# Performance work log

Measured on AMD Instinct MI355X. Metric: run time of the kernel, lower is better.

## Reference

```python
import jax, jax.numpy as jnp
import numpy as np

H, DH, DIM, BNECK, NK, COND = 8, 64, 256, 128, 32, 256


def _ln(x):
    m = x.mean(-1, keepdims=True)
    v = ((x - m) ** 2).mean(-1, keepdims=True)
    return (x - m) * jax.lax.rsqrt(v + 1e-5)


def _mlp(x, w1, b1, w2, b2):
    return jax.nn.gelu(x @ w1 + b1) @ w2 + b2


def _radial(d, w):
    # Bessel-type radial basis sin(n*d)/d projected to heads; limit n as d->0
    n = jnp.arange(1, NK + 1, dtype=d.dtype)
    safe = jnp.maximum(d, 1e-6)[..., None]
    basis = jnp.where(d[..., None] > 1e-6, jnp.sin(d[..., None] * n) / safe, n)
    return jnp.einsum('ijk,kh->hij', basis, w)


def _kernel(x, qk_w):
    # DotProductKernel with softmax=False, scale=1.0
    b, n, _ = x.shape
    qk = (x @ qk_w).reshape(b, n, 2, H, DH).transpose(0, 3, 2, 1, 4)  # b h two n d
    q, k = qk[:, :, 0], qk[:, :, 1]
    return jnp.einsum('bhid,bhjd->bhij', q, k)


def reference(u, lat, lat_diff, lon_diff, scalar_cond, adaLN_w, adaLN_b, to_v_w, to_x_in_w, to_x_w1, to_x_b1, to_x_w2, to_x_b2, to_y_in_w, to_y_w1, to_y_b1, to_y_w2, to_y_b2, kx_qk_w, ky_qk_w, rx_w, ry_w, merge_w, merge_b, ffn_w1, ffn_b1, ffn_w2, ffn_b2):
    b, nlat, nlon, c = u.shape
    mod = (scalar_cond @ adaLN_w + adaLN_b)[:, None, None]  # (b,1,1,6c)
    sh_msa, sc_msa, g_msa, sh_mlp, sc_mlp, g_mlp = jnp.split(mod, 6, axis=-1)
    u_skip = u
    um = _ln(u) * (1 + sc_msa) + sh_msa  # modulate_fused
    lw = jnp.cos(lat)
    lw = lw / lw.mean()
    # PoolingReducer over lat (weighted) -> (b, nlon, bneck)
    u_x = _mlp(jnp.einsum('bilc,cd,i->bld', um, to_x_in_w, lw) / nlat,
               to_x_w1, to_x_b1, to_x_w2, to_x_b2)
    # PoolingReducer over lon -> (b, nlat, bneck)
    u_y = _mlp((um @ to_y_in_w).mean(axis=2), to_y_w1, to_y_b1, to_y_w2, to_y_b2)
    k_x = jax.nn.softmax(_kernel(u_x, kx_qk_w) * _radial(lon_diff, rx_w)[None], axis=-1)
    k_y = jax.nn.softmax(_kernel(u_y, ky_qk_w) * _radial(lat_diff, ry_w)[None], axis=-1)
    v = (um @ to_v_w).reshape(b, nlat, nlon, H, DH).transpose(0, 3, 1, 2, 4)  # b h i l c
    u_phi = jnp.einsum('bhij,bhjmc->bhimc', k_y, v)
    u_phi = jnp.einsum('bhlm,bhimc->bhilc', k_x, u_phi)
    u_phi = u_phi.transpose(0, 2, 3, 1, 4)  # b i l h c
    mu = u_phi.mean(-1, keepdims=True)
    var = ((u_phi - mu) ** 2).mean(-1, keepdims=True)
    gn = ((u_phi - mu) * jax.lax.rsqrt(var + 1e-6)).reshape(b, nlat, nlon, H * DH)
    u1 = u_skip + g_msa * (gn @ merge_w + merge_b)  # bias_dropout_add_scale (inference)
    u2 = _ln(u1) * (1 + sc_mlp) + sh_mlp
    return u1 + g_mlp * _mlp(u2, ffn_w1, ffn_b1, ffn_w2, ffn_b2)


def setup_inputs():
    key = jax.random.key(0)
    ks = jax.random.split(key, 20)
    b, nlat, nlon = 4, 128, 256
    dim, h, dh, bn, cond = DIM, H, DH, BNECK, COND
    f = jnp.float32
    u = jax.random.normal(ks[0], (b, nlat, nlon, dim), f)
    lat = jnp.linspace(-np.pi / 2 + 0.01, np.pi / 2 - 0.01, nlat).astype(f)
    lat_diff = jnp.abs(lat[:, None] - lat[None, :])
    lon = (jnp.arange(nlon) * (2 * np.pi / nlon)).astype(f)
    d = jnp.abs(lon[:, None] - lon[None, :])
    lon_diff = jnp.minimum(d, 2 * np.pi - d)
    scalar_cond = jax.random.normal(ks[1], (b, cond), f)

    def w(k, shape, s=0.02):
        return jax.random.normal(k, shape, f) * s

    return dict(
        u=u, lat=lat, lat_diff=lat_diff, lon_diff=lon_diff, scalar_cond=scalar_cond,
        adaLN_w=w(ks[2], (cond, 6 * dim)), adaLN_b=w(ks[3], (6 * dim,)),
        to_v_w=w(ks[4], (dim, h * dh)),
        to_x_in_w=w(ks[5], (dim, dim)), to_x_w1=w(ks[6], (dim, dim)), to_x_b1=jnp.zeros((dim,), f),
        to_x_w2=w(ks[7], (dim, bn)), to_x_b2=jnp.zeros((bn,), f),
        to_y_in_w=w(ks[8], (dim, dim)), to_y_w1=w(ks[9], (dim, dim)), to_y_b1=jnp.zeros((dim,), f),
        to_y_w2=w(ks[10], (dim, bn)), to_y_b2=jnp.zeros((bn,), f),
        kx_qk_w=w(ks[11], (bn, 2 * h * dh)), ky_qk_w=w(ks[12], (bn, 2 * h * dh)),
        rx_w=w(ks[13], (NK, h), 0.1), ry_w=w(ks[14], (NK, h), 0.1),
        merge_w=w(ks[15], (h * dh, dim)), merge_b=jnp.zeros((dim,), f),
        ffn_w1=w(ks[16], (dim, 4 * dim)), ffn_b1=jnp.zeros((4 * dim,), f),
        ffn_w2=w(ks[17], (4 * dim, dim)), ffn_b2=jnp.zeros((dim,), f))
```

## Files before the change

### kernel.cpp

```cpp
#include <hip/hip_runtime.h>
#include <hip/hip_bf16.h>
#include <math.h>


#define B_ 4
#define NLAT 128
#define NLON 256
#define NTOK (B_*NLAT*NLON)
#define SLOT_ELE ((size_t)16777216)

typedef __hip_bfloat16 bf16;
typedef unsigned short u16;
typedef __attribute__((ext_vector_type(8))) short short8;
typedef __attribute__((ext_vector_type(4))) float f32x4;

__device__ __forceinline__ float b2f(bf16 x){ return __bfloat162float(x); }
__device__ __forceinline__ bf16  f2b(float x){ return __float2bfloat16(x); }
__device__ __forceinline__ u16 f2bits(float x){
  bf16 h = __float2bfloat16(x); return *(u16*)&h;
}
__device__ __forceinline__ float bits2f(u16 u){
  union { unsigned int i; float f; } v; v.i = ((unsigned int)u) << 16; return v.f;
}
__device__ __forceinline__ float gelu_f(float x){
  float x3 = x*x*x;
  return 0.5f*x*(1.0f + tanhf(0.7978845608028654f*(x + 0.044715f*x3)));
}
__device__ __forceinline__ float gelu_fast(float x){
  float t = 0.7978845608028654f*(x + 0.044715f*x*x*x);
  float e = __builtin_amdgcn_exp2f(t * 2.8853900817779268f);
  return x - x*__builtin_amdgcn_rcpf(e + 1.0f);
}
__device__ __forceinline__ float ldin(const void* p, size_t i, int flag){
  return flag ? b2f(((const bf16*)p)[i]) : ((const float*)p)[i];
}
__device__ __forceinline__ short4 pack4(float a, float b, float c, float d){
  short4 r; r.x = (short)f2bits(a); r.y = (short)f2bits(b);
  r.z = (short)f2bits(c); r.w = (short)f2bits(d); return r;
}
__device__ __forceinline__ short8 pack8(float a, float b, float c, float d,
                                        float e, float f, float g, float h){
  short8 r;
  r[0]=(short)f2bits(a); r[1]=(short)f2bits(b); r[2]=(short)f2bits(c); r[3]=(short)f2bits(d);
  r[4]=(short)f2bits(e); r[5]=(short)f2bits(f); r[6]=(short)f2bits(g); r[7]=(short)f2bits(h);
  return r;
}
__device__ __forceinline__ void stage16(const u16* g, u16* l){
  __builtin_amdgcn_global_load_lds(
      (const __attribute__((address_space(1))) void*)g,
      (__attribute__((address_space(3))) void*)l, 16, 0, 0);
}

__global__ void k_detect(const void* lon_diff, int* flag){
  const float c = 0.02454369260617026f;
  float asF = ((const float*)lon_diff)[1];
  float asB = b2f(((const bf16*)lon_diff)[1]);
  float ef = fabsf(asF - c), eb = fabsf(asB - c);
  if (!isfinite(ef)) ef = 1e30f;
  *flag = (eb < ef) ? 1 : 0;
}

struct CvtTab {
  const void* src[27];
  float* dst[27];
  int cum[28];
};
__global__ __launch_bounds__(256) void k_cvtall(CvtTab t, const int* __restrict__ flag,
                                                int total){
  int f = *flag;
  for (int i = blockIdx.x*256 + threadIdx.x; i < total; i += gridDim.x*256){
    int s = 0;
    while (i >= t.cum[s+1]) ++s;
    int off = i - t.cum[s];
    t.dst[s][off] = ldin(t.src[s], off, f);
  }
}

__global__ __launch_bounds__(256) void k_wprep(const float* __restrict__ W,
                                               u16* __restrict__ wf,
                                               int KS, int ldn, int total){
  int gid = blockIdx.x*256 + threadIdx.x;
  if (gid >= total) return;
  int j = gid & 7; int lane = (gid >> 3) & 63; int rest = gid >> 9;
  int ks = rest % KS; int nt = rest / KS;
  int k = ks*32 + (lane >> 4)*8 + j;
  int n = nt*16 + (lane & 15);
  wf[gid] = f2bits(W[(size_t)k*ldn + n]);
}

__global__ __launch_bounds__(256) void k_wprep2(const float* __restrict__ W,
                                                u16* __restrict__ wf){
  int gid = blockIdx.x*256 + threadIdx.x;
  int j = gid & 7; int lane = (gid >> 3) & 63; int rest = gid >> 9;
  int nt = rest & 15; int ksAll = rest >> 4;
  int k = ksAll*32 + (lane >> 4)*8 + j;
  int n = nt*16 + (lane & 15);
  wf[gid] = f2bits(W[(size_t)k*256 + n]);
}

__global__ __launch_bounds__(256) void k_wtrans(const float* __restrict__ W,
                                                u16* __restrict__ WT, int K, int N){
  int gid = blockIdx.x*256 + threadIdx.x;
  if (gid >= K*N) return;
  int k = gid % K, n = gid / K;
  WT[(size_t)n*K + k] = f2bits(W[(size_t)k*N + n]);
}

__global__ __launch_bounds__(256) void k_mod(const float* __restrict__ sc,
                                             const float* __restrict__ w,
                                             const float* __restrict__ bias,
                                             float* __restrict__ mod){
  int gid = blockIdx.x*256 + threadIdx.x;
  int s = gid / 1536, j = gid % 1536;
  float acc = bias[j];
  for (int c = 0; c < 256; ++c) acc += sc[s*256+c] * w[c*1536+j];
  mod[gid] = acc;
}

__global__ __launch_bounds__(128) void k_lw(const float* __restrict__ lat,
                                            float* __restrict__ lw){
  __shared__ float red[128];
  int i = threadIdx.x;
  float cv = cosf(lat[i]);
  red[i] = cv; __syncthreads();
  for (int s = 64; s > 0; s >>= 1){ if (i < s) red[i] += red[i+s]; __syncthreads(); }
  float mean = red[0] * (1.0f/128.0f);
  lw[i] = cv / mean;
}

__global__ __launch_bounds__(256) void k_um2(const void* __restrict__ u,
                                             const float* __restrict__ mod,
                                             u16* __restrict__ um,
                                             const int* __restrict__ flag){
  __shared__ u16 tile[64][264];
  __shared__ float r1[64][4], r2[64][4], mv[64], rs[64];
  __shared__ float ssh[256], ssc[256];
  int f = *flag; int tid = threadIdx.x;
  int t0 = blockIdx.x*64; int b = t0 >> 15;
  ssh[tid] = mod[b*1536 + tid];
  ssc[tid] = mod[b*1536 + 256 + tid];
  for (int it = 0; it < 16; ++it){
    int idx = it*256 + tid;
    int tok = idx >> 6, c4 = idx & 63;
    short4 v4;
    if (f){
      v4 = *(const short4*)((const bf16*)u + ((size_t)(t0+tok))*256 + c4*4);
    } else {
      float4 fv = ((const float4*)u)[((size_t)(t0+tok))*64 + c4];
      v4 = pack4(fv.x, fv.y, fv.z, fv.w);
    }
    *(short4*)&tile[tok][c4*4] = v4;
  }
  __syncthreads();
  {
    int tok = tid >> 2, part = tid & 3;
    float s1 = 0.f, s2 = 0.f;
    for (int c4 = 0; c4 < 16; ++c4){
      short4 v4 = *(const short4*)&tile[tok][part*64 + c4*4];
      float a = bits2f((u16)v4.x), bb = bits2f((u16)v4.y),
            c = bits2f((u16)v4.z), d = bits2f((u16)v4.w);
      s1 += a+bb+c+d; s2 += a*a+bb*bb+c*c+d*d;
    }
    r1[tok][part] = s1; r2[tok][part] = s2;
  }
  __syncthreads();
  if ((tid & 3) == 0){
    int tok = tid >> 2;
    float a1 = r1[tok][0]+r1[tok][1]+r1[tok][2]+r1[tok][3];
    float a2 = r2[tok][0]+r2[tok][1]+r2[tok][2]+r2[tok][3];
    float mean = a1*(1.0f/256.0f);
    float var = a2*(1.0f/256.0f) - mean*mean;
    mv[tok] = mean; rs[tok] = rsqrtf(var + 1e-5f);
  }
  __syncthreads();
  for (int it = 0; it < 16; ++it){
    int idx = it*256 + tid;
    int tok = idx >> 6, c4 = idx & 63;
    float mean = mv[tok], rstd = rs[tok];
    short4 v4 = *(const short4*)&tile[tok][c4*4];
    float y[4]; u16 raw[4] = {(u16)v4.x,(u16)v4.y,(u16)v4.z,(u16)v4.w};
    #pragma unroll
    for (int p = 0; p < 4; ++p){
      int c = c4*4 + p;
      y[p] = (bits2f(raw[p]) - mean)*rstd*(1.0f + ssc[c]) + ssh[c];
    }
    *(short4*)(um + ((size_t)(t0+tok))*256 + c4*4) = pack4(y[0],y[1],y[2],y[3]);
  }
}

__global__ __launch_bounds__(256) void k_redx(const u16* __restrict__ um,
                                              const float* __restrict__ lw,
                                              float* __restrict__ redx){
  __shared__ float lws[128];
  int tid = threadIdx.x;
  if (tid < 128) lws[tid] = lw[tid];
  __syncthreads();
  int gid = blockIdx.x*256 + tid;
  int c = gid & 255; int l = (gid >> 8) & 255; int b = gid >> 16;
  float acc = 0.0f;
  for (int i = 0; i < 128; ++i)
    acc += bits2f(um[(((size_t)(b*128 + i)*256 + l)*256) + c]) * lws[i];
  redx[gid] = acc * (1.0f/128.0f);
}

__global__ __launch_bounds__(256) void k_redy(const u16* __restrict__ um,
                                              float* __restrict__ redy){
  int gid = blockIdx.x*256 + threadIdx.x;
  int c = gid & 255; int i = (gid >> 8) & 127; int b = gid >> 15;
  float acc = 0.0f;
  for (int l = 0; l < 256; ++l)
    acc += bits2f(um[(((size_t)(b*128 + i)*256 + l)*256) + c]);
  redy[gid] = acc * (1.0f/256.0f);
}

__global__ __launch_bounds__(256) void gemm_row2(
    const float* __restrict__ Ax, const float* __restrict__ Wx,
    const float* __restrict__ bx, float* __restrict__ Cx, int Kx, int Nx,
    const float* __restrict__ Ay, const float* __restrict__ Wy,
    const float* __restrict__ by, float* __restrict__ Cy, int Ky, int Ny,
    int nbx, int act){
  __shared__ float As[256];
  int bid = blockIdx.x; int tid = threadIdx.x;
  const float* A; const float* W; const float* bias; float* C; int K, N, r;
  if (bid < nbx){ A=Ax; W=Wx; bias=bx; C=Cx; K=Kx; N=Nx; r=bid; }
  else          { A=Ay; W=Wy; bias=by; C=Cy; K=Ky; N=Ny; r=bid-nbx; }
  for (int k = tid; k < K; k += 256) As[k] = A[(size_t)r*K + k];
  __syncthreads();
  for (int n = tid; n < N; n += 256){
    float a0=0.f, a1=0.f, a2=0.f, a3=0.f;
    for (int k = 0; k < K; k += 4){
      a0 += As[k+0]*W[(size_t)(k+0)*N + n];
      a1 += As[k+1]*W[(size_t)(k+1)*N + n];
      a2 += As[k+2]*W[(size_t)(k+2)*N + n];
      a3 += As[k+3]*W[(size_t)(k+3)*N + n];
    }
    float acc = (a0+a1)+(a2+a3) + (bias ? bias[n] : 0.0f);
    if (act == 1) acc = gelu_f(acc);
    C[(size_t)r*N + n] = acc;
  }
}

__global__ __launch_bounds__(256) void k_radial(const float* __restrict__ d,
                                                const float* __restrict__ w,
                                                float* __restrict__ rad, int n){
  int gid = blockIdx.x*256 + threadIdx.x;
  int nn = n*n;
  int h = gid / nn; int rem = gid % nn;
  float dv = d[rem];
  float safe = fmaxf(dv, 1e-6f);
  float acc = 0.0f;
  for (int k = 0; k < 32; ++k){
    float nk = (float)(k+1);
    float basis = (dv > 1e-6f) ? (sinf(dv*nk)/safe) : nk;
    acc += basis * w[k*8 + h];
  }
  rad[gid] = acc;
}

__global__ __launch_bounds__(256) void k_qkT(const float* __restrict__ qk,
                                             float* __restrict__ kT, int n){
  int gid = blockIdx.x*256 + threadIdx.x;
  int j = gid % n; int rest = gid / n;
  int d = rest & 63; int bh = rest >> 6;
  int b = bh >> 3, h = bh & 7;
  kT[gid] = qk[((size_t)(b*n + j))*1024 + 512 + h*64 + d];
}

__global__ __launch_bounds__(256) void k_attn2(const float* __restrict__ qk,
                                               const float* __restrict__ kT,
                                               const float* __restrict__ rad,
                                               u16* __restrict__ kout, int n){
  extern __shared__ float sm[];
  float* qs = sm; float* red = sm + 64;
  int j = threadIdx.x;
  int bid = blockIdx.x; int i = bid % n; int h = (bid / n) & 7; int b = bid / (n*8);
  if (j < 64) qs[j] = qk[((size_t)(b*n + i))*1024 + h*64 + j];
  __syncthreads();
  const float* kcol = kT + ((size_t)((b*8 + h)*64))*n + j;
  float dot = 0.0f;
  #pragma unroll 8
  for (int d0 = 0; d0 < 64; ++d0) dot += qs[d0]*kcol[(size_t)d0*n];
  float s = dot * rad[((size_t)(h*n + i))*n + j];
  float m = s;
  #pragma unroll
  for (int off = 32; off; off >>= 1) m = fmaxf(m, __shfl_xor(m, off));
  int wv = j >> 6, nw = n >> 6;
  if ((j & 63) == 0) red[wv] = m;
  __syncthreads();
  m = red[0];
  for (int w = 1; w < nw; ++w) m = fmaxf(m, red[w]);
  float e = __builtin_amdgcn_exp2f((s - m)*1.44269504088896f);
  float t = e;
  #pragma unroll
  for (int off = 32; off; off >>= 1) t += __shfl_xor(t, off);
  if ((j & 63) == 0) red[4 + wv] = t;
  __syncthreads();
  t = 0.0f;
  for (int w = 0; w < nw; ++w) t += red[4 + w];
  kout[(size_t)bid*n + j] = f2bits(e / t);
}

__global__ __launch_bounds__(256, 2) void k_v3(const u16* __restrict__ um,
                                               const u16* __restrict__ WvT,
                                               u16* __restrict__ vA,
                                               int b0, size_t bstr){
  __shared__ __align__(16) u16 T[512][72];
  int tid = threadIdx.x;
  int wave = tid>>6, lane = tid&63, quad = lane>>4, l15 = lane&15;
  int bid = blockIdx.x;
  int b = b0 + (bid >> 9);
  int rem = bid & 511;
  int m = rem & 255, jt = rem >> 8;
  const u16* umb = um + ((size_t)b*32768)*256;
  f32x4 acc[8][4];
  #pragma unroll
  for (int mt = 0; mt < 8; ++mt)
    #pragma unroll
    for (int nt = 0; nt < 4; ++nt) acc[mt][nt] = (f32x4){0.f,0.f,0.f,0.f};
  for (int ks = 0; ks < 8; ++ks){
    short8 bfr[4];
    #pragma unroll
    for (int nt = 0; nt < 4; ++nt){
      int j = jt*64 + nt*16 + l15;
      bfr[nt] = *(const short8*)(umb + ((size_t)j*256 + m)*256 + ks*32 + quad*8);
    }
    #pragma unroll
    for (int mt = 0; mt < 8; ++mt){
      short8 a = *(const short8*)(WvT + (size_t)((wave*8+mt)*16 + l15)*256 + ks*32 + quad*8);
      #pragma unroll
      for (int nt = 0; nt < 4; ++nt)
        acc[mt][nt] = __builtin_amdgcn_mfma_f32_16x16x32_bf16(a, bfr[nt], acc[mt][nt], 0, 0, 0);
    }
  }
  #pragma unroll
  for (int mt = 0; mt < 8; ++mt){
    int hc0 = (wave*8+mt)*16 + quad*4;
    #pragma unroll
    for (int nt = 0; nt < 4; ++nt){
      int jp = nt*16 + l15;
      T[hc0+0][jp] = f2bits(acc[mt][nt][0]);
      T[hc0+1][jp] = f2bits(acc[mt][nt][1]);
      T[hc0+2][jp] = f2bits(acc[mt][nt][2]);
      T[hc0+3][jp] = f2bits(acc[mt][nt][3]);
    }
  }
  __syncthreads();
  u16* vAb = vA + (size_t)(b - b0)*bstr;
  for (int it = 0; it < 16; ++it){
    int idx = it*256 + tid;
    int g = idx & 7, hc = idx >> 3;
    short8 v8 = *(const short8*)&T[hc][g*8];
    int h = hc >> 6, c = hc & 63;
    *(short8*)(vAb + (size_t)h*2097152 + ((size_t)c*256 + m)*128 + jt*64 + g*8) = v8;
  }
}

__global__ __launch_bounds__(256) void k_phi1c(const u16* __restrict__ kyb,
                                               const u16* __restrict__ vA,
                                               u16* __restrict__ phi,
                                               int b0, size_t bstr){
  int tid = threadIdx.x;
  int wave = tid>>6, lane = tid&63, quad = lane>>4, l15 = lane&15;
  int bid = blockIdx.x;
  int b = b0 + (bid >> 9);
  int rem = bid & 511; int mblk = rem & 63, h = rem >> 6;
  int m0 = mblk*256;
  const u16* vAh = vA + (size_t)(b - b0)*bstr + (size_t)h*2097152;
  u16* phib = phi + (size_t)(b - b0)*bstr;
  const u16* kyh = kyb + (size_t)(b*8+h)*16384;
  f32x4 acc[4][8];
  #pragma unroll
  for (int mt = 0; mt < 4; ++mt)
    #pragma unroll
    for (int nt = 0; nt < 8; ++nt) acc[mt][nt] = (f32x4){0.f,0.f,0.f,0.f};
  for (int ks = 0; ks < 4; ++ks){
    short8 bfr[8];
    #pragma unroll
    for (int nt = 0; nt < 8; ++nt)
      bfr[nt] = *(const short8*)(kyh + (size_t)(nt*16 + l15)*128 + ks*32 + quad*8);
    #pragma unroll
    for (int mt = 0; mt < 4; ++mt){
      int cm = m0 + (wave*4+mt)*16 + l15;
      short8 a = *(const short8*)(vAh + (size_t)cm*128 + ks*32 + quad*8);
      #pragma unroll
      for (int nt = 0; nt < 8; ++nt)
        acc[mt][nt] = __builtin_amdgcn_mfma_f32_16x16x32_bf16(a, bfr[nt], acc[mt][nt], 0, 0, 0);
    }
  }
  #pragma unroll
  for (int mt = 0; mt < 4; ++mt){
    int cmr = m0 + (wave*4+mt)*16 + quad*4;
    #pragma unroll
    for (int nt = 0; nt < 8; ++nt){
      int i = nt*16 + l15;
      *(short4*)(phib + (size_t)h*2097152 + (size_t)i*16384 + cmr)
        = pack4(acc[mt][nt][0], acc[mt][nt][1], acc[mt][nt][2], acc[mt][nt][3]);
    }
  }
}

__global__ __launch_bounds__(256) void k_phi2b(const u16* __restrict__ kxb,
                                               const u16* __restrict__ phi,
                                               u16* __restrict__ OUTt,
                                               int b0, size_t bstr){
  int tid = threadIdx.x;
  int wave = tid>>6, lane = tid&63, quad = lane>>4, l15 = lane&15;
  int bid = blockIdx.x;
  int b = b0 + (bid >> 9);
  int rem = bid & 511; int mblk = rem & 63, h = rem >> 6;
  int m0 = mblk*128;
  int mhalf = (wave&1)*4, nhalf = (wave>>1)*8;
  const u16* ph = phi + (size_t)(b - b0)*bstr + (size_t)h*2097152;
  u16* OUTb = OUTt + (size_t)(b - b0)*bstr;
  const u16* kxh = kxb + (size_t)(b*8+h)*65536;
  f32x4 acc[4][8];
  #pragma unroll
  for (int mt = 0; mt < 4; ++mt)
    #pragma unroll
    for (int nt = 0; nt < 8; ++nt) acc[mt][nt] = (f32x4){0.f,0.f,0.f,0.f};
  for (int ks = 0; ks < 8; ++ks){
    short8 bfr[8];
    #pragma unroll
    for (int nt = 0; nt < 8; ++nt)
      bfr[nt] = *(const short8*)(kxh + (size_t)((nhalf+nt)*16 + l15)*256 + ks*32 + quad*8);
    #pragma unroll
    for (int mt = 0; mt < 4; ++mt){
      int m2 = m0 + (mhalf+mt)*16 + l15;
      short8 a = *(const short8*)(ph + (size_t)m2*256 + ks*32 + quad*8);
      #pragma unroll
      for (int nt = 0; nt < 8; ++nt)
        acc[mt][nt] = __builtin_amdgcn_mfma_f32_16x16x32_bf16(a, bfr[nt], acc[mt][nt], 0, 0, 0);
    }
  }
  #pragma unroll
  for (int mt = 0; mt < 4; ++mt){
    int m2r = m0 + (mhalf+mt)*16 + quad*4;
    #pragma unroll
    for (int nt = 0; nt < 8; ++nt){
      int l = (nhalf+nt)*16 + l15;
      *(short4*)(OUTb + (size_t)h*2097152 + (size_t)l*8192 + m2r)
        = pack4(acc[mt][nt][0], acc[mt][nt][1], acc[mt][nt][2], acc[mt][nt][3]);
    }
  }
}

__global__ __launch_bounds__(256) void k_gnb(const u16* __restrict__ OUTt,
                                             u16* __restrict__ gn,
                                             int b0, size_t bstr){
  int tid = threadIdx.x;
  int bid = blockIdx.x;
  int bi = bid >> 11;
  int rem = bid & 2047; int l = rem & 255, h = rem >> 8;
  int i = tid >> 1, half = tid & 1;
  const u16* src = OUTt + (size_t)bi*bstr + (size_t)h*2097152 + (size_t)l*8192 + i*64 + half*32;
  float v[32]; float s1 = 0.f, s2 = 0.f;
  #pragma unroll
  for (int c4 = 0; c4 < 8; ++c4){
    short4 v4 = *(const short4*)(src + c4*4);
    v[c4*4+0] = bits2f((u16)v4.x); v[c4*4+1] = bits2f((u16)v4.y);
    v[c4*4+2] = bits2f((u16)v4.z); v[c4*4+3] = bits2f((u16)v4.w);
  }
  #pragma unroll
  for (int c = 0; c < 32; ++c){ s1 += v[c]; s2 += v[c]*v[c]; }
  s1 += __shfl_xor(s1, 1); s2 += __shfl_xor(s2, 1);
  float mean = s1*(1.0f/64.0f);
  float var = s2*(1.0f/64.0f) - mean*mean;
  float rstd = rsqrtf(var + 1e-6f);
  u16* dst = gn + (size_t)bi*bstr + ((size_t)(i*256 + l))*512 + h*64 + half*32;
  #pragma unroll
  for (int c4 = 0; c4 < 8; ++c4)
    *(short4*)(dst + c4*4) = pack4((v[c4*4+0]-mean)*rstd, (v[c4*4+1]-mean)*rstd,
                                   (v[c4*4+2]-mean)*rstd, (v[c4*4+3]-mean)*rstd);
}

__global__ __launch_bounds__(256) void k_mergeb(const u16* __restrict__ gn,
                                                const u16* __restrict__ WmT,
                                                const float* __restrict__ biasm,
                                                const float* __restrict__ mod,
                                                const void* __restrict__ u,
                                                void* __restrict__ outv,
                                                const int* __restrict__ flag,
                                                int b0, size_t bstr){
  __shared__ float smg[256], sbb[256];
  int f = *flag;
  int tid = threadIdx.x;
  int bid = blockIdx.x;
  int b = b0 + (bid >> 8);
  int t0 = (bid & 255)*128;
  smg[tid] = mod[b*1536 + 512 + tid];
  sbb[tid] = biasm[tid];
  __syncthreads();
  int wave = tid>>6, lane = tid&63, quad = lane>>4, l15 = lane&15;
  const u16* gnb = gn + (size_t)(b - b0)*bstr;
  int nt0 = wave*2;
  f32x4 acc[16][2];
  #pragma unroll
  for (int mt = 0; mt < 16; ++mt){ acc[mt][0] = (f32x4){0.f,0.f,0.f,0.f}; acc[mt][1] = (f32x4){0.f,0.f,0.f,0.f}; }
  for (int ks = 0; ks < 16; ++ks){
    short8 bfr[2];
    #pragma unroll
    for (int nti = 0; nti < 2; ++nti){
      int tok = t0 + (nt0+nti)*16 + l15;
      bfr[nti] = *(const short8*)(gnb + (size_t)tok*512 + ks*32 + quad*8);
    }
    #pragma unroll
    for (int mt = 0; mt < 16; ++mt){
      short8 a = *(const short8*)(WmT + (size_t)(mt*16 + l15)*512 + ks*32 + quad*8);
      #pragma unroll
      for (int nti = 0; nti < 2; ++nti)
        acc[mt][nti] = __builtin_amdgcn_mfma_f32_16x16x32_bf16(a, bfr[nti], acc[mt][nti], 0, 0, 0);
    }
  }
  #pragma unroll
  for (int mt = 0; mt < 16; ++mt){
    int d0 = mt*16 + quad*4;
    #pragma unroll
    for (int nti = 0; nti < 2; ++nti){
      int tok = t0 + (nt0+nti)*16 + l15;
      size_t o = ((size_t)b*32768 + tok)*256 + d0;
      float r0,r1,r2,r3;
      if (f){
        short4 rv = *(const short4*)((const bf16*)u + o);
        r0 = bits2f((u16)rv.x); r1 = bits2f((u16)rv.y); r2 = bits2f((u16)rv.z); r3 = bits2f((u16)rv.w);
      } else {
        float4 rv = *(const float4*)((const float*)u + o);
        r0 = rv.x; r1 = rv.y; r2 = rv.z; r3 = rv.w;
      }
      float y0 = r0 + smg[d0+0]*(acc[mt][nti][0] + sbb[d0+0]);
      float y1 = r1 + smg[d0+1]*(acc[mt][nti][1] + sbb[d0+1]);
      float y2 = r2 + smg[d0+2]*(acc[mt][nti][2] + sbb[d0+2]);
      float y3 = r3 + smg[d0+3]*(acc[mt][nti][3] + sbb[d0+3]);
      if (f) *(short4*)((bf16*)outv + o) = pack4(y0,y1,y2,y3);
      else   *(float4*)((float*)outv + o) = (float4){y0,y1,y2,y3};
    }
  }
}

__global__ __launch_bounds__(256, 2) void k_ffn4(
    const float* __restrict__ mod,
    const u16* __restrict__ w1f,
    const float* __restrict__ b1c,
    const u16* __restrict__ w2f,
    const float* __restrict__ b2c,
    void* __restrict__ outv,
    const int* __restrict__ flag){
  __shared__ __align__(16) u16 wbuf[2][16384];
  __shared__ __align__(16) u16 hs[64][40];
  int f = *flag;
  int tid = threadIdx.x;
  int wave = tid>>6, lane = tid&63, quad = lane>>4, l15 = lane&15;
  int mrow = wave*16;
  int t0 = blockIdx.x*64;
  int bb = t0 >> 15;
  const float* modp = mod + bb*1536;
  size_t rowbase = ((size_t)(t0 + mrow + l15))*256;

  {
    #pragma unroll
    for (int i = 0; i < 8; ++i){
      int seg = wave*8 + i;
      const u16* src = (seg < 16)
          ? (w1f + (size_t)seg*512 + lane*8)
          : (w2f + (size_t)(seg-16)*512 + lane*8);
      stage16(src, &wbuf[0][seg*512]);
    }
  }

  short8 afr[8];
  float s1 = 0.f, s2 = 0.f;
  #pragma unroll
  for (int ks = 0; ks < 8; ++ks){
    int c0 = ks*32 + quad*8;
    float v0,v1,v2,v3,v4,v5,v6,v7;
    if (f){
      short8 r = *(const short8*)((const bf16*)outv + rowbase + c0);
      afr[ks] = r;
      v0 = bits2f((u16)r[0]); v1 = bits2f((u16)r[1]); v2 = bits2f((u16)r[2]); v3 = bits2f((u16)r[3]);
      v4 = bits2f((u16)r[4]); v5 = bits2f((u16)r[5]); v6 = bits2f((u16)r[6]); v7 = bits2f((u16)r[7]);
    } else {
      float4 fa = *(const float4*)((const float*)outv + rowbase + c0);
      float4 fb = *(const float4*)((const float*)outv + rowbase + c0 + 4);
      v0=fa.x; v1=fa.y; v2=fa.z; v3=fa.w; v4=fb.x; v5=fb.y; v6=fb.z; v7=fb.w;
      afr[ks] = pack8(v0,v1,v2,v3,v4,v5,v6,v7);
    }
    s1 += v0+v1+v2+v3+v4+v5+v6+v7;
    s2 += v0*v0+v1*v1+v2*v2+v3*v3+v4*v4+v5*v5+v6*v6+v7*v7;
  }
  s1 += __shfl_xor(s1, 16); s1 += __shfl_xor(s1, 32);
  s2 += __shfl_xor(s2, 16); s2 += __shfl_xor(s2, 32);
  float mean = s1*(1.0f/256.0f);
  float var = s2*(1.0f/256.0f) - mean*mean;
  float rstd = rsqrtf(var + 1e-5f);
  #pragma unroll
  for (int ks = 0; ks < 8; ++ks){
    int c0 = ks*32 + quad*8;
    float4 sh0 = *(const float4*)&modp[768 + c0];
    float4 sh1 = *(const float4*)&modp[768 + c0 + 4];
    float4 sc0 = *(const float4*)&modp[1024 + c0];
    float4 sc1 = *(const float4*)&modp[1024 + c0 + 4];
    short8 r = afr[ks];
    float y0 = (bits2f((u16)r[0]) - mean)*rstd*(1.0f+sc0.x) + sh0.x;
    float y1 = (bits2f((u16)r[1]) - mean)*rstd*(1.0f+sc0.y) + sh0.y;
    float y2 = (bits2f((u16)r[2]) - mean)*rstd*(1.0f+sc0.z) + sh0.z;
    float y3 = (bits2f((u16)r[3]) - mean)*rstd*(1.0f+sc0.w) + sh0.w;
    float y4 = (bits2f((u16)r[4]) - mean)*rstd*(1.0f+sc1.x) + sh1.x;
    float y5 = (bits2f((u16)r[5]) - mean)*rstd*(1.0f+sc1.y) + sh1.y;
    float y6 = (bits2f((u16)r[6]) - mean)*rstd*(1.0f+sc1.z) + sh1.z;
    float y7 = (bits2f((u16)r[7]) - mean)*rstd*(1.0f+sc1.w) + sh1.w;
    afr[ks] = pack8(y0,y1,y2,y3,y4,y5,y6,y7);
  }

  __syncthreads();

  f32x4 acc2[16];
  #pragma unroll
  for (int nt = 0; nt < 16; ++nt) acc2[nt] = (f32x4){0.f,0.f,0.f,0.f};
  int buf = 0;
  #pragma unroll 1
  for (int c = 0; c < 32; ++c){
    if (c < 31){
      int cn = c + 1;
      #pragma unroll
      for (int i = 0; i < 8; ++i){
        int seg = wave*8 + i;
        const u16* src = (seg < 16)
            ? (w1f + (size_t)cn*8192 + (size_t)seg*512 + lane*8)
            : (w2f + (size_t)cn*8192 + (size_t)(seg-16)*512 + lane*8);
        stage16(src, &wbuf[buf^1][seg*512]);
      }
    }
    const u16* w1l = &wbuf[buf][0];
    const u16* w2l = &wbuf[buf][8192];
    f32x4 acc1[2];
    acc1[0] = (f32x4){0.f,0.f,0.f,0.f}; acc1[1] = (f32x4){0.f,0.f,0.f,0.f};
    #pragma unroll
    for (int ks = 0; ks < 8; ++ks){
      #pragma unroll
      for (int nt2 = 0; nt2 < 2; ++nt2){
        short8 bfr = *(const short8*)(w1l + (nt2*8 + ks)*512 + lane*8);
        acc1[nt2] = __builtin_amdgcn_mfma_f32_16x16x32_bf16(afr[ks], bfr, acc1[nt2], 0, 0, 0);
      }
    }
    __builtin_amdgcn_sched_barrier(0);
    #pragma unroll
    for (int nt2 = 0; nt2 < 2; ++nt2){
      int hid = nt2*16 + l15;
      float b1 = b1c[c*32 + hid];
      #pragma unroll
      for (int r = 0; r < 4; ++r)
        hs[mrow + quad*4 + r][hid] = f2bits(gelu_fast(acc1[nt2][r] + b1));
    }
    __builtin_amdgcn_sched_barrier(0);
    asm volatile("s_waitcnt lgkmcnt(0)" ::: "memory");
    __builtin_amdgcn_sched_barrier(0);
    short8 a2 = *(const short8*)&hs[mrow + l15][quad*8];
    #pragma unroll
    for (int nt = 0; nt < 16; ++nt){
      short8 bfr = *(const short8*)(w2l + nt*512 + lane*8);
      acc2[nt] = __builtin_amdgcn_mfma_f32_16x16x32_bf16(a2, bfr, acc2[nt], 0, 0, 0);
    }
    __syncthreads();
    buf ^= 1;
  }

  #pragma unroll
  for (int nt = 0; nt < 16; ++nt){
    int col = nt*16 + l15;
    float g = modp[1280 + col];
    float b2v = b2c[col];
    #pragma unroll
    for (int r = 0; r < 4; ++r){
      size_t o = ((size_t)(t0 + mrow + quad*4 + r))*256 + col;
      float resid = f ? bits2f(((const u16*)outv)[o]) : ((const float*)outv)[o];
      float y = resid + g*(acc2[nt][r] + b2v);
      if (f) ((u16*)outv)[o] = f2bits(y);
      else   ((float*)outv)[o] = y;
    }
  }
}

extern "C" void kernel_launch(void* const* d_in, const int* in_sizes, int n_in,
                              void* d_out, int out_size, void* d_ws, size_t ws_size,
                              hipStream_t stream){
  (void)n_in; (void)out_size;

  char* p = (char*)d_ws;
  auto alloc = [&](size_t bytes)->void*{
    void* r = (void*)p; p += (bytes + 255) & ~(size_t)255; return r;
  };

  int* flag = (int*)alloc(4);
  float* cin[28];
  cin[0] = nullptr;
  for (int i = 1; i < 28; ++i) cin[i] = (float*)alloc((size_t)in_sizes[i]*4);

  float* mod  = (float*)alloc((size_t)4*1536*4);
  float* lw   = (float*)alloc((size_t)128*4);
  float* redx = (float*)alloc((size_t)4*256*256*4);
  float* redy = (float*)alloc((size_t)4*128*256*4);
  float* tx   = (float*)alloc((size_t)4*256*256*4);
  float* hx   = (float*)alloc((size_t)4*256*256*4);
  float* uxb  = (float*)alloc((size_t)4*256*128*4);
  float* ty   = (float*)alloc((size_t)4*128*256*4);
  float* hy   = (float*)alloc((size_t)4*128*256*4);
  float* uyb  = (float*)alloc((size_t)4*128*128*4);
  float* qkx  = (float*)alloc((size_t)4*256*1024*4);
  float* qky  = (float*)alloc((size_t)4*128*1024*4);
  float* kTx  = (float*)alloc((size_t)4*8*64*256*4);
  float* kTy  = (float*)alloc((size_t)4*8*64*128*4);
  float* radx = (float*)alloc((size_t)8*256*256*4);
  float* rady = (float*)alloc((size_t)8*128*128*4);
  u16* kxb = (u16*)alloc((size_t)32*256*256*2);
  u16* kyb = (u16*)alloc((size_t)32*128*128*2);
  u16* w1f = (u16*)alloc((size_t)256*1024*2);
  u16* w2f = (u16*)alloc((size_t)1024*256*2);
  u16* WvT = (u16*)alloc((size_t)512*256*2);
  u16* WmT = (u16*)alloc((size_t)256*512*2);
  u16* um  = (u16*)alloc((size_t)NTOK*256*2);

  size_t used = (size_t)(p - (char*)d_ws);
  int merged = (ws_size > used) && ((ws_size - used) >= (size_t)8*SLOT_ELE*2 + 65536);
  size_t slotBytes = (merged ? 4 : 1) * SLOT_ELE * 2;
  u16* slotV = (u16*)alloc(slotBytes);
  u16* slotP = (u16*)alloc(slotBytes);

  const void* u = d_in[0];

  k_detect<<<1, 1, 0, stream>>>(d_in[3], flag);
  {
    CvtTab t;
    int cum = 0;
    for (int i = 1; i < 28; ++i){
      t.src[i-1] = d_in[i];
      t.dst[i-1] = cin[i];
      t.cum[i-1] = cum;
      cum += in_sizes[i];
    }
    t.cum[27] = cum;
    k_cvtall<<<2048, 256, 0, stream>>>(t, flag, cum);
  }
  k_wprep<<<1024, 256, 0, stream>>>(cin[24], w1f, 8, 1024, 256*1024);
  k_wprep2<<<1024, 256, 0, stream>>>(cin[26], w2f);
  k_wtrans<<<512, 256, 0, stream>>>(cin[7],  WvT, 256, 512);
  k_wtrans<<<512, 256, 0, stream>>>(cin[22], WmT, 512, 256);

  k_mod<<<24, 256, 0, stream>>>(cin[4], cin[5], cin[6], mod);
  k_lw<<<1, 128, 0, stream>>>(cin[1], lw);
  k_um2<<<NTOK/64, 256, 0, stream>>>(u, mod, um, flag);
  k_redx<<<1024, 256, 0, stream>>>(um, lw, redx);
  k_redy<<<512, 256, 0, stream>>>(um, redy);
  gemm_row2<<<1536, 256, 0, stream>>>(redx, cin[8],  nullptr,  tx,  256, 256,
                                      redy, cin[13], nullptr,  ty,  256, 256, 1024, 0);
  gemm_row2<<<1536, 256, 0, stream>>>(tx,   cin[9],  cin[10],  hx,  256, 256,
                                      ty,   cin[14], cin[15],  hy,  256, 256, 1024, 1);
  gemm_row2<<<1536, 256, 0, stream>>>(hx,   cin[11], cin[12],  uxb, 256, 128,
                                      hy,   cin[16], cin[17],  uyb, 256, 128, 1024, 0);
  gemm_row2<<<1536, 256, 0, stream>>>(uxb,  cin[18], nullptr,  qkx, 128, 1024,
                                      uyb,  cin[19], nullptr,  qky, 128, 1024, 1024, 0);
  k_radial<<<(8*256*256)/256, 256, 0, stream>>>(cin[3], cin[20], radx, 256);
  k_radial<<<(8*128*128)/256, 256, 0, stream>>>(cin[2], cin[21], rady, 128);
  k_qkT<<<2048, 256, 0, stream>>>(qkx, kTx, 256);
  k_qkT<<<1024, 256, 0, stream>>>(qky, kTy, 128);
  k_attn2<<<4*8*256, 256, (64+8)*4, stream>>>(qkx, kTx, radx, kxb, 256);
  k_attn2<<<4*8*128, 128, (64+8)*4, stream>>>(qky, kTy, rady, kyb, 128);

  if (merged){
    k_v3    <<<2048, 256, 0, stream>>>(um, WvT, slotV, 0, SLOT_ELE);
    k_phi1c <<<2048, 256, 0, stream>>>(kyb, slotV, slotP, 0, SLOT_ELE);
    k_phi2b <<<2048, 256, 0, stream>>>(kxb, slotP, slotV, 0, SLOT_ELE);
    k_gnb   <<<8192, 256, 0, stream>>>(slotV, slotP, 0, SLOT_ELE);
    k_mergeb<<<1024, 256, 0, stream>>>(slotP, WmT, cin[23], mod, u, d_out, flag, 0, SLOT_ELE);
  } else {
    for (int b = 0; b < 4; ++b){
      k_v3    <<<512, 256, 0, stream>>>(um, WvT, slotV, b, 0);
      k_phi1c <<<512, 256, 0, stream>>>(kyb, slotV, slotP, b, 0);
      k_phi2b <<<512, 256, 0, stream>>>(kxb, slotP, slotV, b, 0);
      k_gnb   <<<2048, 256, 0, stream>>>(slotV, slotP, b, 0);
      k_mergeb<<<256, 256, 0, stream>>>(slotP, WmT, cin[23], mod, u, d_out, flag, b, 0);
    }
  }
  k_ffn4<<<NTOK/64, 256, 0, stream>>>(mod, w1f, cin[25], w2f, cin[27], d_out, flag);
}
```

Baseline: 1.452 ms.

## Fuse reductions and bottleneck MLP chain, tile K transpose, restructure FFN second GEMM

Merges the lat/lon pooling reductions into one launch and folds the four row-wise GEMMs (input projection, MLP, qk projection) into a single per-row kernel that keeps intermediates in shared memory, removing launches and global round-trips. The K transpose now goes through a shared-memory tile for coalesced reads and writes. In the FFN kernel's second GEMM, each wave now computes a 4x4 tile over all 64 token rows and a column slice instead of 16 rows by all columns, which adds a block barrier before the shared activations are read. The fused bottleneck kernel runs serially through four dependent matvecs per row, so it is latency-bound.

New measurement: 1.726 ms. +18.8%, slower.

```diff
diff --git a/kernel.cpp b/kernel.cpp
--- a/kernel.cpp
+++ b/kernel.cpp
@@ -188,55 +188,97 @@
   }
 }
 
-__global__ __launch_bounds__(256) void k_redx(const u16* __restrict__ um,
-                                              const float* __restrict__ lw,
-                                              float* __restrict__ redx){
+__global__ __launch_bounds__(256) void k_redxy(const u16* __restrict__ um,
+                                               const float* __restrict__ lw,
+                                               float* __restrict__ redx,
+                                               float* __restrict__ redy){
   __shared__ float lws[128];
   int tid = threadIdx.x;
   if (tid < 128) lws[tid] = lw[tid];
   __syncthreads();
   int gid = blockIdx.x*256 + tid;
-  int c = gid & 255; int l = (gid >> 8) & 255; int b = gid >> 16;
-  float acc = 0.0f;
-  for (int i = 0; i < 128; ++i)
-    acc += bits2f(um[(((size_t)(b*128 + i)*256 + l)*256) + c]) * lws[i];
-  redx[gid] = acc * (1.0f/128.0f);
-}
-
-__global__ __launch_bounds__(256) void k_redy(const u16* __restrict__ um,
-                                              float* __restrict__ redy){
-  int gid = blockIdx.x*256 + threadIdx.x;
-  int c = gid & 255; int i = (gid >> 8) & 127; int b = gid >> 15;
-  float acc = 0.0f;
-  for (int l = 0; l < 256; ++l)
-    acc += bits2f(um[(((size_t)(b*128 + i)*256 + l)*256) + c]);
-  redy[gid] = acc * (1.0f/256.0f);
-}
-
-__global__ __launch_bounds__(256) void gemm_row2(
-    const float* __restrict__ Ax, const float* __restrict__ Wx,
-    const float* __restrict__ bx, float* __restrict__ Cx, int Kx, int Nx,
-    const float* __restrict__ Ay, const float* __restrict__ Wy,
-    const float* __restrict__ by, float* __restrict__ Cy, int Ky, int Ny,
-    int nbx, int act){
-  __shared__ float As[256];
+  if (gid < 262144){
+    int c = gid & 255; int l = (gid >> 8) & 255; int b = gid >> 16;
+    float acc = 0.0f;
+    for (int i = 0; i < 128; ++i)
+      acc += bits2f(um[(((size_t)(b*128 + i)*256 + l)*256) + c]) * lws[i];
+    redx[gid] = acc * (1.0f/128.0f);
+  } else {
+    int g = gid - 262144;
+    int c = g & 255; int i = (g >> 8) & 127; int b = g >> 15;
+    float acc = 0.0f;
+    for (int l = 0; l < 256; ++l)
+      acc += bits2f(um[(((size_t)(b*128 + i)*256 + l)*256) + c]);
+    redy[g] = acc * (1.0f/256.0f);
+  }
+}
+
+__global__ __launch_bounds__(256) void k_bneck(
+    const float* __restrict__ Ax, const float* __restrict__ Winx,
+    const float* __restrict__ W1x, const float* __restrict__ b1x,
+    const float* __restrict__ W2x, const float* __restrict__ b2x,
+    const float* __restrict__ Wqx, float* __restrict__ Qx,
+    const float* __restrict__ Ay, const float* __restrict__ Winy,
+    const float* __restrict__ W1y, const float* __restrict__ b1y,
+    const float* __restrict__ W2y, const float* __restrict__ b2y,
+    const float* __restrict__ Wqy, float* __restrict__ Qy,
+    int nbx){
+  __shared__ float s0[256], s1[256], s2[128];
   int bid = blockIdx.x; int tid = threadIdx.x;
-  const float* A; const float* W; const float* bias; float* C; int K, N, r;
-  if (bid < nbx){ A=Ax; W=Wx; bias=bx; C=Cx; K=Kx; N=Nx; r=bid; }
-  else          { A=Ay; W=Wy; bias=by; C=Cy; K=Ky; N=Ny; r=bid-nbx; }
-  for (int k = tid; k < K; k += 256) As[k] = A[(size_t)r*K + k];
-  __syncthreads();
-  for (int n = tid; n < N; n += 256){
-    float a0=0.f, a1=0.f, a2=0.f, a3=0.f;
-    for (int k = 0; k < K; k += 4){
-      a0 += As[k+0]*W[(size_t)(k+0)*N + n];
-      a1 += As[k+1]*W[(size_t)(k+1)*N + n];
-      a2 += As[k+2]*W[(size_t)(k+2)*N + n];
-      a3 += As[k+3]*W[(size_t)(k+3)*N + n];
-    }
-    float acc = (a0+a1)+(a2+a3) + (bias ? bias[n] : 0.0f);
-    if (act == 1) acc = gelu_f(acc);
-    C[(size_t)r*N + n] = acc;
+  const float *A, *Win, *W1, *b1, *W2, *b2, *Wq; float* Q; int r;
+  if (bid < nbx){ A=Ax; Win=Winx; W1=W1x; b1=b1x; W2=W2x; b2=b2x; Wq=Wqx; Q=Qx; r=bid; }
+  else          { A=Ay; Win=Winy; W1=W1y; b1=b1y; W2=W2y; b2=b2y; Wq=Wqy; Q=Qy; r=bid-nbx; }
+  s0[tid] = A[(size_t)r*256 + tid];
+  __syncthreads();
+  {
+    float a0=0.f,a1=0.f,a2=0.f,a3=0.f;
+    for (int k = 0; k < 256; k += 4){
+      a0 += s0[k+0]*Win[(size_t)(k+0)*256 + tid];
+      a1 += s0[k+1]*Win[(size_t)(k+1)*256 + tid];
+      a2 += s0[k+2]*Win[(size_t)(k+2)*256 + tid];
+      a3 += s0[k+3]*Win[(size_t)(k+3)*256 + tid];
+    }
+    __syncthreads();
+    s1[tid] = (a0+a1)+(a2+a3);
+    __syncthreads();
+  }
+  {
+    float a0=0.f,a1=0.f,a2=0.f,a3=0.f;
+    for (int k = 0; k < 256; k += 4){
+      a0 += s1[k+0]*W1[(size_t)(k+0)*256 + tid];
+      a1 += s1[k+1]*W1[(size_t)(k+1)*256 + tid];
+      a2 += s1[k+2]*W1[(size_t)(k+2)*256 + tid];
+      a3 += s1[k+3]*W1[(size_t)(k+3)*256 + tid];
+    }
+    __syncthreads();
+    s0[tid] = gelu_f((a0+a1)+(a2+a3) + b1[tid]);
+    __syncthreads();
+  }
+  {
+    float a0=0.f,a1=0.f,a2=0.f,a3=0.f;
+    if (tid < 128){
+      for (int k = 0; k < 256; k += 4){
+        a0 += s0[k+0]*W2[(size_t)(k+0)*128 + tid];
+        a1 += s0[k+1]*W2[(size_t)(k+1)*128 + tid];
+        a2 += s0[k+2]*W2[(size_t)(k+2)*128 + tid];
+        a3 += s0[k+3]*W2[(size_t)(k+3)*128 + tid];
+      }
+    }
+    __syncthreads();
+    if (tid < 128) s2[tid] = (a0+a1)+(a2+a3) + b2[tid];
+    __syncthreads();
+  }
+  #pragma unroll
+  for (int p = 0; p < 4; ++p){
+    int n = p*256 + tid;
+    float a0=0.f,a1=0.f,a2=0.f,a3=0.f;
+    for (int k = 0; k < 128; k += 4){
+      a0 += s2[k+0]*Wq[(size_t)(k+0)*1024 + n];
+      a1 += s2[k+1]*Wq[(size_t)(k+1)*1024 + n];
+      a2 += s2[k+2]*Wq[(size_t)(k+2)*1024 + n];
+      a3 += s2[k+3]*Wq[(size_t)(k+3)*1024 + n];
+    }
+    Q[(size_t)r*1024 + n] = (a0+a1)+(a2+a3);
   }
 }
 
@@ -257,13 +299,25 @@
   rad[gid] = acc;
 }
 
-__global__ __launch_bounds__(256) void k_qkT(const float* __restrict__ qk,
-                                             float* __restrict__ kT, int n){
-  int gid = blockIdx.x*256 + threadIdx.x;
-  int j = gid % n; int rest = gid / n;
-  int d = rest & 63; int bh = rest >> 6;
-  int b = bh >> 3, h = bh & 7;
-  kT[gid] = qk[((size_t)(b*n + j))*1024 + 512 + h*64 + d];
+__global__ __launch_bounds__(256) void k_qkT2(const float* __restrict__ qk,
+                                              float* __restrict__ kT, int n){
+  __shared__ float tile[64][65];
+  int tid = threadIdx.x;
+  int bid = blockIdx.x;
+  int ntj = n >> 6;
+  int jt = bid % ntj; int h = (bid / ntj) & 7; int b = bid / (ntj*8);
+  int j0 = jt*64;
+  for (int it = 0; it < 16; ++it){
+    int idx = it*256 + tid;
+    int jr = idx >> 6, d = idx & 63;
+    tile[jr][d] = qk[((size_t)(b*n + j0 + jr))*1024 + 512 + h*64 + d];
+  }
+  __syncthreads();
+  for (int it = 0; it < 16; ++it){
+    int idx = it*256 + tid;
+    int dr = idx >> 6, j = idx & 63;
+    kT[((size_t)((b*8 + h)*64 + dr))*n + j0 + j] = tile[j][dr];
+  }
 }
 
 __global__ __launch_bounds__(256) void k_attn2(const float* __restrict__ qk,
@@ -536,7 +590,7 @@
   }
 }
 
-__global__ __launch_bounds__(256, 2) void k_ffn4(
+__global__ __launch_bounds__(256, 2) void k_ffn6(
     const float* __restrict__ mod,
     const u16* __restrict__ w1f,
     const float* __restrict__ b1c,
@@ -612,9 +666,11 @@
 
   __syncthreads();
 
-  f32x4 acc2[16];
-  #pragma unroll
-  for (int nt = 0; nt < 16; ++nt) acc2[nt] = (f32x4){0.f,0.f,0.f,0.f};
+  f32x4 acc2[4][4];
+  #pragma unroll
+  for (int tt = 0; tt < 4; ++tt)
+    #pragma unroll
+    for (int ct = 0; ct < 4; ++ct) acc2[tt][ct] = (f32x4){0.f,0.f,0.f,0.f};
   int buf = 0;
   #pragma unroll 1
   for (int c = 0; c < 32; ++c){
@@ -652,30 +708,38 @@
     }
     __builtin_amdgcn_sched_barrier(0);
     asm volatile("s_waitcnt lgkmcnt(0)" ::: "memory");
+    __builtin_amdgcn_s_barrier();
     __builtin_amdgcn_sched_barrier(0);
-    short8 a2 = *(const short8*)&hs[mrow + l15][quad*8];
-    #pragma unroll
-    for (int nt = 0; nt < 16; ++nt){
-      short8 bfr = *(const short8*)(w2l + nt*512 + lane*8);
-      acc2[nt] = __builtin_amdgcn_mfma_f32_16x16x32_bf16(a2, bfr, acc2[nt], 0, 0, 0);
+    short8 a2[4];
+    #pragma unroll
+    for (int tt = 0; tt < 4; ++tt)
+      a2[tt] = *(const short8*)&hs[tt*16 + l15][quad*8];
+    #pragma unroll
+    for (int ct = 0; ct < 4; ++ct){
+      short8 bfr = *(const short8*)(w2l + (wave*4 + ct)*512 + lane*8);
+      #pragma unroll
+      for (int tt = 0; tt < 4; ++tt)
+        acc2[tt][ct] = __builtin_amdgcn_mfma_f32_16x16x32_bf16(a2[tt], bfr, acc2[tt][ct], 0, 0, 0);
     }
     __syncthreads();
     buf ^= 1;
   }
 
   #pragma unroll
-  for (int nt = 0; nt < 16; ++nt){
-    int col = nt*16 + l15;
+  for (int ct = 0; ct < 4; ++ct){
+    int col = (wave*4 + ct)*16 + l15;
     float g = modp[1280 + col];
     float b2v = b2c[col];
     #pragma unroll
-    for (int r = 0; r < 4; ++r){
-      size_t o = ((size_t)(t0 + mrow + quad*4 + r))*256 + col;
-      float resid = f ? bits2f(((const u16*)outv)[o]) : ((const float*)outv)[o];
-      float y = resid + g*(acc2[nt][r] + b2v);
-      if (f) ((u16*)outv)[o] = f2bits(y);
-      else   ((float*)outv)[o] = y;
-    }
+    for (int tt = 0; tt < 4; ++tt)
+      #pragma unroll
+      for (int r = 0; r < 4; ++r){
+        size_t o = ((size_t)(t0 + tt*16 + quad*4 + r))*256 + col;
+        float resid = f ? bits2f(((const u16*)outv)[o]) : ((const float*)outv)[o];
+        float y = resid + g*(acc2[tt][ct][r] + b2v);
+        if (f) ((u16*)outv)[o] = f2bits(y);
+        else   ((float*)outv)[o] = y;
+      }
   }
 }
 
@@ -698,12 +762,6 @@
   float* lw   = (float*)alloc((size_t)128*4);
   float* redx = (float*)alloc((size_t)4*256*256*4);
   float* redy = (float*)alloc((size_t)4*128*256*4);
-  float* tx   = (float*)alloc((size_t)4*256*256*4);
-  float* hx   = (float*)alloc((size_t)4*256*256*4);
-  float* uxb  = (float*)alloc((size_t)4*256*128*4);
-  float* ty   = (float*)alloc((size_t)4*128*256*4);
-  float* hy   = (float*)alloc((size_t)4*128*256*4);
-  float* uyb  = (float*)alloc((size_t)4*128*128*4);
   float* qkx  = (float*)alloc((size_t)4*256*1024*4);
   float* qky  = (float*)alloc((size_t)4*128*1024*4);
   float* kTx  = (float*)alloc((size_t)4*8*64*256*4);
@@ -747,20 +805,14 @@
   k_mod<<<24, 256, 0, stream>>>(cin[4], cin[5], cin[6], mod);
   k_lw<<<1, 128, 0, stream>>>(cin[1], lw);
   k_um2<<<NTOK/64, 256, 0, stream>>>(u, mod, um, flag);
-  k_redx<<<1024, 256, 0, stream>>>(um, lw, redx);
-  k_redy<<<512, 256, 0, stream>>>(um, redy);
-  gemm_row2<<<1536, 256, 0, stream>>>(redx, cin[8],  nullptr,  tx,  256, 256,
-                                      redy, cin[13], nullptr,  ty,  256, 256, 1024, 0);
-  gemm_row2<<<1536, 256, 0, stream>>>(tx,   cin[9],  cin[10],  hx,  256, 256,
-                                      ty,   cin[14], cin[15],  hy,  256, 256, 1024, 1);
-  gemm_row2<<<1536, 256, 0, stream>>>(hx,   cin[11], cin[12],  uxb, 256, 128,
-                                      hy,   cin[16], cin[17],  uyb, 256, 128, 1024, 0);
-  gemm_row2<<<1536, 256, 0, stream>>>(uxb,  cin[18], nullptr,  qkx, 128, 1024,
-                                      uyb,  cin[19], nullptr,  qky, 128, 1024, 1024, 0);
+  k_redxy<<<1536, 256, 0, stream>>>(um, lw, redx, redy);
+  k_bneck<<<1536, 256, 0, stream>>>(
+      redx, cin[8],  cin[9],  cin[10], cin[11], cin[12], cin[18], qkx,
+      redy, cin[13], cin[14], cin[15], cin[16], cin[17], cin[19], qky, 1024);
   k_radial<<<(8*256*256)/256, 256, 0, stream>>>(cin[3], cin[20], radx, 256);
   k_radial<<<(8*128*128)/256, 256, 0, stream>>>(cin[2], cin[21], rady, 128);
-  k_qkT<<<2048, 256, 0, stream>>>(qkx, kTx, 256);
-  k_qkT<<<1024, 256, 0, stream>>>(qky, kTy, 128);
+  k_qkT2<<<4*8*4, 256, 0, stream>>>(qkx, kTx, 256);
+  k_qkT2<<<4*8*2, 256, 0, stream>>>(qky, kTy, 128);
   k_attn2<<<4*8*256, 256, (64+8)*4, stream>>>(qkx, kTx, radx, kxb, 256);
   k_attn2<<<4*8*128, 128, (64+8)*4, stream>>>(qky, kTy, rady, kyb, 128);
 
@@ -779,5 +831,5 @@
       k_mergeb<<<256, 256, 0, stream>>>(slotP, WmT, cin[23], mod, u, d_out, flag, b, 0);
     }
   }
-  k_ffn4<<<NTOK/64, 256, 0, stream>>>(mod, w1f, cin[25], w2f, cin[27], d_out, flag);
-}
+  k_ffn6<<<NTOK/64, 256, 0, stream>>>(mod, w1f, cin[25], w2f, cin[27], d_out, flag);
+}
```
